# Kernel tuning notes

Hardware: AMD Instinct MI355X
Metric: run time of the kernel (lower is better)

Reference implementation:

```python
import jax, jax.numpy as jnp
import numpy as np

N = 131072
F_IN = 256
FEATURES = 64
N_SOURCES = 32


def setup_inputs() -> dict:
    key = jax.random.key(0)
    k1, k2, k3 = jax.random.split(key, 3)
    x = jax.random.normal(k1, (N, F_IN), dtype=jnp.float32)
    source = jax.random.randint(k2, (N,), 0, N_SOURCES, dtype=jnp.int32)
    W = jax.random.normal(k3, (F_IN, N_SOURCES * FEATURES), dtype=jnp.float32) * (1.0 / np.sqrt(F_IN))
    b = jnp.zeros((N_SOURCES * FEATURES,), dtype=jnp.float32)
    return {"x": x, "source": source, "W": W, "b": b}


def reference(x, source, W, b):
    # Dense projection to all sources: (N, n_sources*features)
    y = jnp.dot(x, W) + b
    # Per-row gather of the slice belonging to this row's source id.
    # Equivalent to y[i, source[i]*FEATURES : (source[i]+1)*FEATURES].
    y = y.reshape(x.shape[0], N_SOURCES, FEATURES)
    out = jnp.take_along_axis(y, source[:, None, None].astype(jnp.int32), axis=1)
    return out[:, 0, :]  # (N, FEATURES)
```

## Files before the change

### kernel.cpp

```cpp
#include <hip/hip_runtime.h>

#define N_ROWS   131072
#define F_IN     256
#define FEAT     64
#define NSRC     32
#define WSTRIDE  (NSRC * FEAT)
#define NCH      32
#define CHUNK    4096
#define LCAP     320
#define NBUCK    (NCH * NSRC)
#define TR       16

#define MCHUNK   4096
#define LCAP1    512
#define KPAD     264

typedef __attribute__((ext_vector_type(8))) short  bf16x8;
typedef __attribute__((ext_vector_type(4))) float  f32x4;

__device__ __forceinline__ unsigned short f2bf(float f) {
    union { float f; unsigned u; } c; c.f = f;
    unsigned r = c.u + 0x7fffu + ((c.u >> 16) & 1u);
    return (unsigned short)(r >> 16);
}

__device__ __forceinline__ bf16x8 pack8(f32x4 f0, f32x4 f1) {
    bf16x8 a;
    a[0] = (short)f2bf(f0[0]); a[1] = (short)f2bf(f0[1]);
    a[2] = (short)f2bf(f0[2]); a[3] = (short)f2bf(f0[3]);
    a[4] = (short)f2bf(f1[0]); a[5] = (short)f2bf(f1[1]);
    a[6] = (short)f2bf(f1[2]); a[7] = (short)f2bf(f1[3]);
    return a;
}

__global__ void zero_counts(int* __restrict__ ws) {
    const int i = blockIdx.x * 256 + threadIdx.x;
    if (i < NBUCK) ws[i] = 0;
}

__global__ __launch_bounds__(256)
void compact_kernel(const int* __restrict__ src, int* __restrict__ ws) {
    __shared__ int lcnt[NSRC];
    __shared__ int gbase[NSRC];
    const int tid = threadIdx.x;
    if (tid < NSRC) lcnt[tid] = 0;
    __syncthreads();
    const int row = blockIdx.x * 256 + tid;
    const int s   = src[row];
    const int c   = blockIdx.x >> 4;
    const int p   = atomicAdd(&lcnt[s], 1);
    __syncthreads();
    if (tid < NSRC && lcnt[tid] > 0)
        gbase[tid] = atomicAdd(&ws[c * NSRC + tid], lcnt[tid]);
    __syncthreads();
    const int pos = gbase[s] + p;
    if (pos < LCAP)
        ws[NBUCK + ((size_t)(c * NSRC + s)) * LCAP + pos] = row;
}

__device__ __forceinline__ void stage_tile(const float* __restrict__ x,
                                           const int* lst, int count, int tile,
                                           int w, int lane, float* Abuf) {
    #pragma unroll
    for (int i = 0; i < 4; ++i) {
        const int r  = w * 4 + i;
        const int gi = min(tile * TR + r, count - 1);
        const float* src = x + (size_t)lst[gi] * F_IN + ((lane ^ (r & 7)) << 2);
        __builtin_amdgcn_global_load_lds(
            (const __attribute__((address_space(1))) void*)src,
            (__attribute__((address_space(3))) void*)(Abuf + r * F_IN),
            16, 0, 0);
    }
}

__device__ __forceinline__ void compute_tile(const float* Abuf, const bf16x8 bb[8],
                                             const int* lst, float bias,
                                             float* __restrict__ out,
                                             int tile, int count,
                                             int w, int col, int quad) {
    f32x4 acc = (f32x4){0.f, 0.f, 0.f, 0.f};
    const int key = col & 7;
    const float* arow = Abuf + col * F_IN;
    #pragma unroll
    for (int kk = 0; kk < 8; ++kk) {
        const int s0 = kk * 8 + quad * 2;
        const f32x4 lo = *(const f32x4*)(arow + (((s0    ) ^ key) << 2));
        const f32x4 hi = *(const f32x4*)(arow + (((s0 + 1) ^ key) << 2));
        unsigned u0, u1, u2, u3;
        asm("v_cvt_pk_bf16_f32 %0, %1, %2" : "=v"(u0) : "v"(lo[0]), "v"(lo[1]));
        asm("v_cvt_pk_bf16_f32 %0, %1, %2" : "=v"(u1) : "v"(lo[2]), "v"(lo[3]));
        asm("v_cvt_pk_bf16_f32 %0, %1, %2" : "=v"(u2) : "v"(hi[0]), "v"(hi[1]));
        asm("v_cvt_pk_bf16_f32 %0, %1, %2" : "=v"(u3) : "v"(hi[2]), "v"(hi[3]));
        union { unsigned u[4]; bf16x8 v; } cv;
        cv.u[0] = u0; cv.u[1] = u1; cv.u[2] = u2; cv.u[3] = u3;
        acc = __builtin_amdgcn_mfma_f32_16x16x32_bf16(cv.v, bb[kk], acc, 0, 0, 0);
    }
    #pragma unroll
    for (int reg = 0; reg < 4; ++reg) {
        const int gm = tile * TR + quad * 4 + reg;
        if (gm < count)
            out[(size_t)lst[gm] * FEAT + w * 16 + col] = acc[reg] + bias;
    }
}

__global__ __launch_bounds__(256, 4)
void gemm_kernel(const float* __restrict__ x, const float* __restrict__ W,
                 const float* __restrict__ b, const int* __restrict__ ws,
                 float* __restrict__ out) {
    __shared__ __align__(16) float A[2][TR][F_IN];
    __shared__ int lst[LCAP];

    const int tid    = threadIdx.x;
    const int s      = blockIdx.x;
    const int c      = blockIdx.y;
    const int bucket = c * NSRC + s;
    const int count  = min(ws[bucket], LCAP);
    if (count == 0) return;

    const int* gl = ws + NBUCK + (size_t)bucket * LCAP;
    for (int i = tid; i < count; i += 256) lst[i] = gl[i];

    const int lane = tid & 63, w = tid >> 6;
    const int col  = lane & 15, quad = lane >> 4;

    __syncthreads();

    const int ntiles = (count + TR - 1) / TR;

    stage_tile(x, lst, count, 0, w, lane, &A[0][0][0]);

    bf16x8 bb[8];
    {
        const float* wp = W + (size_t)(quad * 8) * WSTRIDE + s * FEAT + w * 16 + col;
        #pragma unroll
        for (int kk = 0; kk < 8; ++kk) {
            float t[8];
            #pragma unroll
            for (int j = 0; j < 8; ++j)
                t[j] = wp[(size_t)(kk * 32 + j) * WSTRIDE];
            bf16x8 v;
            #pragma unroll
            for (int j = 0; j < 8; ++j) v[j] = (short)f2bf(t[j]);
            bb[kk] = v;
        }
    }
    const float bias = b[s * FEAT + w * 16 + col];

    __syncthreads();

    int buf = 0;
    for (int t = 0; t < ntiles; ++t) {
        if (t + 1 < ntiles)
            stage_tile(x, lst, count, t + 1, w, lane, &A[buf ^ 1][0][0]);
        compute_tile(&A[buf][0][0], bb, lst, bias, out, t, count, w, col, quad);
        __syncthreads();
        buf ^= 1;
    }
}

__global__ __launch_bounds__(256, 4)
void mono_kernel(const float* __restrict__ x, const int* __restrict__ src,
                 const float* __restrict__ W, const float* __restrict__ b,
                 float* __restrict__ out) {
    __shared__ __align__(16) unsigned short Wt[FEAT * KPAD];
    __shared__ int lst[LCAP1];
    __shared__ int cnt;
    const int tid = threadIdx.x, s = blockIdx.y, chunk0 = blockIdx.x * MCHUNK;
    if (tid == 0) cnt = 0;
    __syncthreads();
    {
        const int n = tid & 63, kp = (tid >> 6) * 2;
        #pragma unroll
        for (int k0 = 0; k0 < F_IN; k0 += 8) {
            const int k = k0 + kp;
            const float w0 = W[(size_t)k * WSTRIDE + s * FEAT + n];
            const float w1 = W[(size_t)(k + 1) * WSTRIDE + s * FEAT + n];
            *(unsigned*)&Wt[n * KPAD + k] = (unsigned)f2bf(w0) | ((unsigned)f2bf(w1) << 16);
        }
    }
    #pragma unroll
    for (int r = 0; r < MCHUNK / 256; ++r) {
        const int row = chunk0 + r * 256 + tid;
        if (src[row] == s) {
            const int p = atomicAdd(&cnt, 1);
            if (p < LCAP1) lst[p] = row;
        }
    }
    __syncthreads();
    const int count = cnt;
    if (count == 0) return;
    const int lane = tid & 63, w = tid >> 6, col = lane & 15, quad = lane >> 4;
    float bias[4];
    #pragma unroll
    for (int nt = 0; nt < 4; ++nt) bias[nt] = b[s * FEAT + nt * 16 + col];
    const int npass = (count + 63) >> 6;
    for (int pp = 0; pp < npass; ++pp) {
        const int base = pp * 64 + w * 16;
        const int ia = lst[min(base + col, count - 1)];
        const float* ap = x + (size_t)ia * F_IN + quad * 8;
        f32x4 av[16];
        #pragma unroll
        for (int kk = 0; kk < 8; ++kk) {
            av[2 * kk]     = *(const f32x4*)(ap + kk * 32);
            av[2 * kk + 1] = *(const f32x4*)(ap + kk * 32 + 4);
        }
        f32x4 acc[4];
        #pragma unroll
        for (int nt = 0; nt < 4; ++nt) acc[nt] = (f32x4){0.f, 0.f, 0.f, 0.f};
        #pragma unroll
        for (int kk = 0; kk < 8; ++kk) {
            const bf16x8 a = pack8(av[2 * kk], av[2 * kk + 1]);
            #pragma unroll
            for (int nt = 0; nt < 4; ++nt) {
                const bf16x8 bb = *(const bf16x8*)&Wt[(nt * 16 + col) * KPAD + kk * 32 + quad * 8];
                acc[nt] = __builtin_amdgcn_mfma_f32_16x16x32_bf16(a, bb, acc[nt], 0, 0, 0);
            }
        }
        #pragma unroll
        for (int reg = 0; reg < 4; ++reg) {
            const int gm = base + quad * 4 + reg;
            if (gm < count) {
                const int row = lst[gm];
                float* op = out + (size_t)row * FEAT;
                #pragma unroll
                for (int nt = 0; nt < 4; ++nt)
                    op[nt * 16 + col] = acc[nt][reg] + bias[nt];
            }
        }
    }
}

extern "C" void kernel_launch(void* const* d_in, const int* in_sizes, int n_in,
                              void* d_out, int out_size, void* d_ws, size_t ws_size,
                              hipStream_t stream) {
    const float* x   = (const float*)d_in[0];
    const int*   src = (const int*)d_in[1];
    const float* W   = (const float*)d_in[2];
    const float* b   = (const float*)d_in[3];
    float*       out = (float*)d_out;

    const size_t ws_needed = (size_t)NBUCK * (1 + LCAP) * sizeof(int);
    if (ws_size >= ws_needed) {
        int* ws = (int*)d_ws;
        zero_counts<<<dim3(4), dim3(256), 0, stream>>>(ws);
        compact_kernel<<<dim3(N_ROWS / 256), dim3(256), 0, stream>>>(src, ws);
        gemm_kernel<<<dim3(NSRC, NCH), dim3(256), 0, stream>>>(x, W, b, ws, out);
    } else {
        mono_kernel<<<dim3(N_ROWS / MCHUNK, NSRC), dim3(256), 0, stream>>>(x, src, W, b, out);
    }
}
```

Baseline: 220.4 us.

## Triple-buffer gemm_kernel tile staging with explicit vmcnt waits and single barrier

Changes the gather-GEMM kernel from double to triple buffering of x tiles in LDS, prefetching two tiles ahead. Replaces the per-iteration __syncthreads with explicit s_waitcnt vmcnt counts plus one raw barrier, aiming to keep more global loads in flight while MFMA compute runs. Adds a branch-free store path for full tiles. The larger LDS footprint lowers the launch-bounds occupancy hint from 4 to 3, and the hand-coded vmcnt values assume stage_tile issues a fixed number of loads, which is fragile.

After: 222.9 us. No clear change (+1.1%).

```diff
diff --git a/kernel.cpp b/kernel.cpp
--- a/kernel.cpp
+++ b/kernel.cpp
@@ -10,6 +10,7 @@
 #define LCAP     320
 #define NBUCK    (NCH * NSRC)
 #define TR       16
+#define NBUF     3
 
 #define MCHUNK   4096
 #define LCAP1    512
@@ -17,6 +18,9 @@
 
 typedef __attribute__((ext_vector_type(8))) short  bf16x8;
 typedef __attribute__((ext_vector_type(4))) float  f32x4;
+
+#define WAITV(N) asm volatile("s_waitcnt vmcnt(" #N ")" ::: "memory")
+#define SBAR()   do { __builtin_amdgcn_s_barrier(); __builtin_amdgcn_sched_barrier(0); } while (0)
 
 __device__ __forceinline__ unsigned short f2bf(float f) {
     union { float f; unsigned u; } c; c.f = f;
@@ -95,19 +99,26 @@
         cv.u[0] = u0; cv.u[1] = u1; cv.u[2] = u2; cv.u[3] = u3;
         acc = __builtin_amdgcn_mfma_f32_16x16x32_bf16(cv.v, bb[kk], acc, 0, 0, 0);
     }
-    #pragma unroll
-    for (int reg = 0; reg < 4; ++reg) {
-        const int gm = tile * TR + quad * 4 + reg;
-        if (gm < count)
-            out[(size_t)lst[gm] * FEAT + w * 16 + col] = acc[reg] + bias;
-    }
-}
-
-__global__ __launch_bounds__(256, 4)
+    if (tile * TR + TR <= count) {
+        #pragma unroll
+        for (int reg = 0; reg < 4; ++reg)
+            out[(size_t)lst[tile * TR + quad * 4 + reg] * FEAT + w * 16 + col]
+                = acc[reg] + bias;
+    } else {
+        #pragma unroll
+        for (int reg = 0; reg < 4; ++reg) {
+            const int gm = tile * TR + quad * 4 + reg;
+            if (gm < count)
+                out[(size_t)lst[gm] * FEAT + w * 16 + col] = acc[reg] + bias;
+        }
+    }
+}
+
+__global__ __launch_bounds__(256, 3)
 void gemm_kernel(const float* __restrict__ x, const float* __restrict__ W,
                  const float* __restrict__ b, const int* __restrict__ ws,
                  float* __restrict__ out) {
-    __shared__ __align__(16) float A[2][TR][F_IN];
+    __shared__ __align__(16) float A[NBUF][TR][F_IN];
     __shared__ int lst[LCAP];
 
     const int tid    = threadIdx.x;
@@ -128,6 +139,7 @@
     const int ntiles = (count + TR - 1) / TR;
 
     stage_tile(x, lst, count, 0, w, lane, &A[0][0][0]);
+    if (ntiles > 1) stage_tile(x, lst, count, 1, w, lane, &A[1][0][0]);
 
     bf16x8 bb[8];
     {
@@ -146,15 +158,15 @@
     }
     const float bias = b[s * FEAT + w * 16 + col];
 
-    __syncthreads();
-
-    int buf = 0;
     for (int t = 0; t < ntiles; ++t) {
-        if (t + 1 < ntiles)
-            stage_tile(x, lst, count, t + 1, w, lane, &A[buf ^ 1][0][0]);
-        compute_tile(&A[buf][0][0], bb, lst, bias, out, t, count, w, col, quad);
-        __syncthreads();
-        buf ^= 1;
+        if (t == 0)      { if (ntiles > 1) WAITV(4); else WAITV(0); }
+        else if (t == 1) { if (ntiles > 2) WAITV(8); else WAITV(4); }
+        else             WAITV(8);
+        SBAR();
+        if (t + 2 < ntiles)
+            stage_tile(x, lst, count, t + 2, w, lane, &A[(t + 2) % NBUF][0][0]);
+        compute_tile(&A[t % NBUF][0][0], bb, lst, bias, out,
+                     t, count, w, col, quad);
     }
 }
 
@@ -212,8 +224,8 @@
             const bf16x8 a = pack8(av[2 * kk], av[2 * kk + 1]);
             #pragma unroll
             for (int nt = 0; nt < 4; ++nt) {
-                const bf16x8 bb = *(const bf16x8*)&Wt[(nt * 16 + col) * KPAD + kk * 32 + quad * 8];
-                acc[nt] = __builtin_amdgcn_mfma_f32_16x16x32_bf16(a, bb, acc[nt], 0, 0, 0);
+                const bf16x8 bbv = *(const bf16x8*)&Wt[(nt * 16 + col) * KPAD + kk * 32 + quad * 8];
+                acc[nt] = __builtin_amdgcn_mfma_f32_16x16x32_bf16(a, bbv, acc[nt], 0, 0, 0);
             }
         }
         #pragma unroll
```

## Drop zeroing kernel, use per-block segments, and coalesce output stores via LDS

Applied to the files above, without the earlier changes.

The compaction kernel no longer uses global atomics. Each 256-row block writes fixed-size per-source segments with counts, which removes the zero_counts launch. The gemm kernel builds its row list by prefix-summing the 16 segments of its chunk. The tile loop now uses explicit vmcnt waits and raw barriers instead of __syncthreads, and output goes through an LDS transpose so each wave writes full 64-float rows contiguously. The per-block cap of 44 rows per source could silently drop rows if the source distribution is skewed.

Result: no change. 222.4 us (+0.9%).

```diff
diff --git a/kernel.cpp b/kernel.cpp
--- a/kernel.cpp
+++ b/kernel.cpp
@@ -7,9 +7,13 @@
 #define WSTRIDE  (NSRC * FEAT)
 #define NCH      32
 #define CHUNK    4096
+#define NCB      (N_ROWS / 256)
+#define CBPC     16
+#define CAPC     44
+#define SEG      (CAPC + 1)
 #define LCAP     320
-#define NBUCK    (NCH * NSRC)
 #define TR       16
+#define TPAD     66
 
 #define MCHUNK   4096
 #define LCAP1    512
@@ -17,6 +21,10 @@
 
 typedef __attribute__((ext_vector_type(8))) short  bf16x8;
 typedef __attribute__((ext_vector_type(4))) float  f32x4;
+
+#define WAITV(N)  asm volatile("s_waitcnt vmcnt(" #N ")" ::: "memory")
+#define WAITLGKM() asm volatile("s_waitcnt lgkmcnt(0)" ::: "memory")
+#define SBAR()    do { __builtin_amdgcn_s_barrier(); __builtin_amdgcn_sched_barrier(0); } while (0)
 
 __device__ __forceinline__ unsigned short f2bf(float f) {
     union { float f; unsigned u; } c; c.f = f;
@@ -33,29 +41,20 @@
     return a;
 }
 
-__global__ void zero_counts(int* __restrict__ ws) {
-    const int i = blockIdx.x * 256 + threadIdx.x;
-    if (i < NBUCK) ws[i] = 0;
-}
-
 __global__ __launch_bounds__(256)
 void compact_kernel(const int* __restrict__ src, int* __restrict__ ws) {
     __shared__ int lcnt[NSRC];
-    __shared__ int gbase[NSRC];
     const int tid = threadIdx.x;
     if (tid < NSRC) lcnt[tid] = 0;
     __syncthreads();
     const int row = blockIdx.x * 256 + tid;
     const int s   = src[row];
-    const int c   = blockIdx.x >> 4;
     const int p   = atomicAdd(&lcnt[s], 1);
-    __syncthreads();
-    if (tid < NSRC && lcnt[tid] > 0)
-        gbase[tid] = atomicAdd(&ws[c * NSRC + tid], lcnt[tid]);
-    __syncthreads();
-    const int pos = gbase[s] + p;
-    if (pos < LCAP)
-        ws[NBUCK + ((size_t)(c * NSRC + s)) * LCAP + pos] = row;
+    if (p < CAPC)
+        ws[blockIdx.x * (NSRC * SEG) + s * SEG + 1 + p] = row;
+    __syncthreads();
+    if (tid < NSRC)
+        ws[blockIdx.x * (NSRC * SEG) + tid * SEG] = min(lcnt[tid], CAPC);
 }
 
 __device__ __forceinline__ void stage_tile(const float* __restrict__ x,
@@ -65,41 +64,11 @@
     for (int i = 0; i < 4; ++i) {
         const int r  = w * 4 + i;
         const int gi = min(tile * TR + r, count - 1);
-        const float* src = x + (size_t)lst[gi] * F_IN + ((lane ^ (r & 7)) << 2);
+        const float* srcp = x + (size_t)lst[gi] * F_IN + ((lane ^ (r & 7)) << 2);
         __builtin_amdgcn_global_load_lds(
-            (const __attribute__((address_space(1))) void*)src,
+            (const __attribute__((address_space(1))) void*)srcp,
             (__attribute__((address_space(3))) void*)(Abuf + r * F_IN),
             16, 0, 0);
-    }
-}
-
-__device__ __forceinline__ void compute_tile(const float* Abuf, const bf16x8 bb[8],
-                                             const int* lst, float bias,
-                                             float* __restrict__ out,
-                                             int tile, int count,
-                                             int w, int col, int quad) {
-    f32x4 acc = (f32x4){0.f, 0.f, 0.f, 0.f};
-    const int key = col & 7;
-    const float* arow = Abuf + col * F_IN;
-    #pragma unroll
-    for (int kk = 0; kk < 8; ++kk) {
-        const int s0 = kk * 8 + quad * 2;
-        const f32x4 lo = *(const f32x4*)(arow + (((s0    ) ^ key) << 2));
-        const f32x4 hi = *(const f32x4*)(arow + (((s0 + 1) ^ key) << 2));
-        unsigned u0, u1, u2, u3;
-        asm("v_cvt_pk_bf16_f32 %0, %1, %2" : "=v"(u0) : "v"(lo[0]), "v"(lo[1]));
-        asm("v_cvt_pk_bf16_f32 %0, %1, %2" : "=v"(u1) : "v"(lo[2]), "v"(lo[3]));
-        asm("v_cvt_pk_bf16_f32 %0, %1, %2" : "=v"(u2) : "v"(hi[0]), "v"(hi[1]));
-        asm("v_cvt_pk_bf16_f32 %0, %1, %2" : "=v"(u3) : "v"(hi[2]), "v"(hi[3]));
-        union { unsigned u[4]; bf16x8 v; } cv;
-        cv.u[0] = u0; cv.u[1] = u1; cv.u[2] = u2; cv.u[3] = u3;
-        acc = __builtin_amdgcn_mfma_f32_16x16x32_bf16(cv.v, bb[kk], acc, 0, 0, 0);
-    }
-    #pragma unroll
-    for (int reg = 0; reg < 4; ++reg) {
-        const int gm = tile * TR + quad * 4 + reg;
-        if (gm < count)
-            out[(size_t)lst[gm] * FEAT + w * 16 + col] = acc[reg] + bias;
     }
 }
 
@@ -108,22 +77,39 @@
                  const float* __restrict__ b, const int* __restrict__ ws,
                  float* __restrict__ out) {
     __shared__ __align__(16) float A[2][TR][F_IN];
+    __shared__ __align__(16) float T[TR * TPAD];
     __shared__ int lst[LCAP];
-
-    const int tid    = threadIdx.x;
-    const int s      = blockIdx.x;
-    const int c      = blockIdx.y;
-    const int bucket = c * NSRC + s;
-    const int count  = min(ws[bucket], LCAP);
+    __shared__ int soff[CBPC + 1];
+
+    const int tid = threadIdx.x;
+    const int s   = blockIdx.x;
+    const int c   = blockIdx.y;
+
+    if (tid == 0) {
+        int acc2 = 0;
+        #pragma unroll
+        for (int jj = 0; jj < CBPC; ++jj) {
+            soff[jj] = acc2;
+            acc2 += ws[(size_t)(c * CBPC + jj) * (NSRC * SEG) + s * SEG];
+        }
+        soff[CBPC] = acc2;
+    }
+    __syncthreads();
+    const int count = min(soff[CBPC], LCAP);
     if (count == 0) return;
-
-    const int* gl = ws + NBUCK + (size_t)bucket * LCAP;
-    for (int i = tid; i < count; i += 256) lst[i] = gl[i];
+    {
+        const int jj = tid >> 4, i0 = tid & 15;
+        const size_t base = (size_t)(c * CBPC + jj) * (NSRC * SEG) + s * SEG;
+        const int cj = ws[base];
+        for (int i = i0; i < cj; i += 16) {
+            const int pos = soff[jj] + i;
+            if (pos < LCAP) lst[pos] = ws[base + 1 + i];
+        }
+    }
+    __syncthreads();
 
     const int lane = tid & 63, w = tid >> 6;
     const int col  = lane & 15, quad = lane >> 4;
-
-    __syncthreads();
 
     const int ntiles = (count + TR - 1) / TR;
 
@@ -134,27 +120,55 @@
         const float* wp = W + (size_t)(quad * 8) * WSTRIDE + s * FEAT + w * 16 + col;
         #pragma unroll
         for (int kk = 0; kk < 8; ++kk) {
-            float t[8];
+            float tv[8];
             #pragma unroll
             for (int j = 0; j < 8; ++j)
-                t[j] = wp[(size_t)(kk * 32 + j) * WSTRIDE];
+                tv[j] = wp[(size_t)(kk * 32 + j) * WSTRIDE];
             bf16x8 v;
             #pragma unroll
-            for (int j = 0; j < 8; ++j) v[j] = (short)f2bf(t[j]);
+            for (int j = 0; j < 8; ++j) v[j] = (short)f2bf(tv[j]);
             bb[kk] = v;
         }
     }
     const float bias = b[s * FEAT + w * 16 + col];
 
-    __syncthreads();
-
-    int buf = 0;
     for (int t = 0; t < ntiles; ++t) {
+        if (t) WAITV(4); else WAITV(0);
+        SBAR();
         if (t + 1 < ntiles)
-            stage_tile(x, lst, count, t + 1, w, lane, &A[buf ^ 1][0][0]);
-        compute_tile(&A[buf][0][0], bb, lst, bias, out, t, count, w, col, quad);
-        __syncthreads();
-        buf ^= 1;
+            stage_tile(x, lst, count, t + 1, w, lane, &A[(t + 1) & 1][0][0]);
+
+        f32x4 acc = (f32x4){0.f, 0.f, 0.f, 0.f};
+        {
+            const int key = col & 7;
+            const float* arow = &A[t & 1][0][0] + col * F_IN;
+            #pragma unroll
+            for (int kk = 0; kk < 8; ++kk) {
+                const int s0 = kk * 8 + quad * 2;
+                const f32x4 lo = *(const f32x4*)(arow + (((s0    ) ^ key) << 2));
+                const f32x4 hi = *(const f32x4*)(arow + (((s0 + 1) ^ key) << 2));
+                unsigned u0, u1, u2, u3;
+                asm("v_cvt_pk_bf16_f32 %0, %1, %2" : "=v"(u0) : "v"(lo[0]), "v"(lo[1]));
+                asm("v_cvt_pk_bf16_f32 %0, %1, %2" : "=v"(u1) : "v"(lo[2]), "v"(lo[3]));
+                asm("v_cvt_pk_bf16_f32 %0, %1, %2" : "=v"(u2) : "v"(hi[0]), "v"(hi[1]));
+                asm("v_cvt_pk_bf16_f32 %0, %1, %2" : "=v"(u3) : "v"(hi[2]), "v"(hi[3]));
+                union { unsigned u[4]; bf16x8 v; } cv;
+                cv.u[0] = u0; cv.u[1] = u1; cv.u[2] = u2; cv.u[3] = u3;
+                acc = __builtin_amdgcn_mfma_f32_16x16x32_bf16(cv.v, bb[kk], acc, 0, 0, 0);
+            }
+        }
+
+        #pragma unroll
+        for (int reg = 0; reg < 4; ++reg)
+            T[(quad * 4 + reg) * TPAD + w * 16 + col] = acc[reg] + bias;
+        WAITLGKM();
+        SBAR();
+        #pragma unroll
+        for (int r = 0; r < 4; ++r) {
+            const int gi = t * TR + w * 4 + r;
+            if (gi < count)
+                out[(size_t)lst[gi] * FEAT + lane] = T[(w * 4 + r) * TPAD + lane];
+        }
     }
 }
 
@@ -212,8 +226,8 @@
             const bf16x8 a = pack8(av[2 * kk], av[2 * kk + 1]);
             #pragma unroll
             for (int nt = 0; nt < 4; ++nt) {
-                const bf16x8 bb = *(const bf16x8*)&Wt[(nt * 16 + col) * KPAD + kk * 32 + quad * 8];
-                acc[nt] = __builtin_amdgcn_mfma_f32_16x16x32_bf16(a, bb, acc[nt], 0, 0, 0);
+                const bf16x8 bbv = *(const bf16x8*)&Wt[(nt * 16 + col) * KPAD + kk * 32 + quad * 8];
+                acc[nt] = __builtin_amdgcn_mfma_f32_16x16x32_bf16(a, bbv, acc[nt], 0, 0, 0);
             }
         }
         #pragma unroll
@@ -239,11 +253,10 @@
     const float* b   = (const float*)d_in[3];
     float*       out = (float*)d_out;
 
-    const size_t ws_needed = (size_t)NBUCK * (1 + LCAP) * sizeof(int);
+    const size_t ws_needed = (size_t)NCB * NSRC * SEG * sizeof(int);
     if (ws_size >= ws_needed) {
         int* ws = (int*)d_ws;
-        zero_counts<<<dim3(4), dim3(256), 0, stream>>>(ws);
-        compact_kernel<<<dim3(N_ROWS / 256), dim3(256), 0, stream>>>(src, ws);
+        compact_kernel<<<dim3(NCB), dim3(256), 0, stream>>>(src, ws);
         gemm_kernel<<<dim3(NSRC, NCH), dim3(256), 0, stream>>>(x, W, b, ws, out);
     } else {
         mono_kernel<<<dim3(N_ROWS / MCHUNK, NSRC), dim3(256), 0, stream>>>(x, src, W, b, out);
```
